# Optimization experiments

Hardware: AMD Instinct MI355X
Metric: run time of the kernel (lower is better)

## Reference

```python
import jax, jax.numpy as jnp
import numpy as np

N = 100000
E = 1600000
F_IN = 64
DIM = 64
OUT = 10
NUM_GRAPHS = 1000
BN_EPS = 1e-5


def gcn_conv(x, W, b, src, dst, n):
    # PyG GCNConv: add self-loops, symmetric normalization, scatter-add.
    h = x @ W                                   # [N, dim]
    ones = jnp.ones(src.shape[0], dtype=x.dtype)
    deg = jax.ops.segment_sum(ones, dst, num_segments=n) + 1.0  # +1 self-loop
    dinv = jax.lax.rsqrt(deg)                   # deg^{-1/2}
    msg = h[src] * (dinv[src] * dinv[dst])[:, None]  # [E, dim]
    out = jax.ops.segment_sum(msg, dst, num_segments=n)
    out = out + h * (dinv * dinv)[:, None]      # self-loop term
    return out + b


def batchnorm_eval(x, gamma, beta, mean, var):
    return (x - mean) * jax.lax.rsqrt(var + BN_EPS) * gamma + beta


def setup_inputs() -> dict:
    key = jax.random.key(0)
    ks = jax.random.split(key, 16)
    x = jax.random.normal(ks[0], (N, F_IN), dtype=jnp.float32)
    edge_index = jax.random.randint(ks[1], (2, E), 0, N)
    batch = jnp.sort(jax.random.randint(ks[2], (N,), 0, NUM_GRAPHS))

    def lin(k, fan_in, fan_out):
        s = 1.0 / np.sqrt(fan_in)
        kw, kb = jax.random.split(k)
        W = jax.random.uniform(kw, (fan_in, fan_out), minval=-s, maxval=s, dtype=jnp.float32)
        b = jax.random.uniform(kb, (fan_out,), minval=-s, maxval=s, dtype=jnp.float32)
        return W, b

    W1, b1 = lin(ks[3], F_IN, DIM)
    W2, b2 = lin(ks[4], DIM, DIM)
    W3, b3 = lin(ks[5], DIM, DIM)
    W4, b4 = lin(ks[6], DIM, DIM)
    lin1_W, lin1_b = lin(ks[7], 4 * DIM, DIM)
    lin2_W, lin2_b = lin(ks[8], DIM, OUT)

    bn_gamma = jnp.ones((4, DIM), dtype=jnp.float32)
    bn_beta = jnp.zeros((4, DIM), dtype=jnp.float32)
    bn_mean = jnp.zeros((4, DIM), dtype=jnp.float32)
    bn_var = jnp.ones((4, DIM), dtype=jnp.float32)

    return {
        'x': x, 'edge_index': edge_index, 'batch': batch, 'num_graphs': NUM_GRAPHS,
        'W1': W1, 'b1': b1, 'W2': W2, 'b2': b2, 'W3': W3, 'b3': b3, 'W4': W4, 'b4': b4,
        'bn_gamma': bn_gamma, 'bn_beta': bn_beta, 'bn_mean': bn_mean, 'bn_var': bn_var,
        'lin1_W': lin1_W, 'lin1_b': lin1_b, 'lin2_W': lin2_W, 'lin2_b': lin2_b,
    }


def reference(x, edge_index, batch, num_graphs, W1, b1, W2, b2, W3, b3, W4, b4,
              bn_gamma, bn_beta, bn_mean, bn_var, lin1_W, lin1_b, lin2_W, lin2_b):
    src, dst = edge_index[0], edge_index[1]
    n = x.shape[0]
    Ws = [(W1, b1), (W2, b2), (W3, b3), (W4, b4)]
    xs = []
    h = x
    for i, (W, b) in enumerate(Ws):
        h = gcn_conv(h, W, b, src, dst, n)
        h = batchnorm_eval(h, bn_gamma[i], bn_beta[i], bn_mean[i], bn_var[i])
        h = jax.nn.relu(h)
        xs.append(h)
    h = jnp.concatenate(xs, axis=-1)                         # JK 'cat' -> [N, 4*dim]
    pooled = jax.ops.segment_sum(h, batch, num_segments=num_graphs)  # [G, 4*dim]
    # dropout is identity in eval mode
    out = jax.nn.relu(pooled @ lin1_W + lin1_b)
    out = out @ lin2_W + lin2_b
    return out
```

## Files before the change

kernel.cpp:

```cpp
#include <hip/hip_runtime.h>
#include <hip/hip_bf16.h>

#define N_NODES   100000
#define N_EDGES   1600000
#define DIM       64
#define OUT_DIM   10
#define N_GRAPHS  1000
#define BN_EPS    1e-5f
#define NBUCKET   391
#define TILE_E    6400
#define NT        250

typedef __hip_bfloat16 bf16;
__device__ __forceinline__ float b2f(bf16 v) { return __bfloat162float(v); }

typedef __attribute__((ext_vector_type(8))) short short8;
typedef __attribute__((ext_vector_type(4))) float floatx4;

__device__ __forceinline__ short f2bs(float f) {
    union { bf16 h; short s; } u;
    u.h = __float2bfloat16(f);
    return u.s;
}


__global__ void __launch_bounds__(256) k_bucket_count(const int* __restrict__ dst,
                                                      int* __restrict__ tileCnt, int e) {
    __shared__ int hcnt[NBUCKET];
    int t = blockIdx.x, tid = threadIdx.x;
    for (int b = tid; b < NBUCKET; b += 256) hcnt[b] = 0;
    __syncthreads();
    int ibase = t * TILE_E;
    for (int j = 0; j < TILE_E; j += 256) {
        int i = ibase + j + tid;
        if (i < e) atomicAdd(&hcnt[dst[i] >> 8], 1);
    }
    __syncthreads();
    for (int b = tid; b < NBUCKET; b += 256) tileCnt[b * NT + t] = hcnt[b];
}


__global__ void __launch_bounds__(256) k_tile_scan(int* __restrict__ tileCnt,
                                                   int* __restrict__ bucketTot) {
    __shared__ int tmp[256];
    int b = blockIdx.x, tid = threadIdx.x;
    int v = (tid < NT) ? tileCnt[b * NT + tid] : 0;
    tmp[tid] = v;
    __syncthreads();
    for (int off = 1; off < 256; off <<= 1) {
        int t = (tid >= off) ? tmp[tid - off] : 0;
        __syncthreads();
        tmp[tid] += t;
        __syncthreads();
    }
    if (tid < NT) tileCnt[b * NT + tid] = tmp[tid] - v;
    if (tid == 255) bucketTot[b] = tmp[255];
}


__global__ void k_scan_sums(int* __restrict__ bsums, int nb) {
    __shared__ int tmp[512];
    int tid = threadIdx.x;
    int v = (tid < nb) ? bsums[tid] : 0;
    tmp[tid] = v;
    __syncthreads();
    for (int off = 1; off < 512; off <<= 1) {
        int t = (tid >= off) ? tmp[tid - off] : 0;
        __syncthreads();
        tmp[tid] += t;
        __syncthreads();
    }
    if (tid < nb) bsums[tid] = tmp[tid] - v;
}


__global__ void __launch_bounds__(256) k_bucket_write(
    const int* __restrict__ src, const int* __restrict__ dst,
    const int* __restrict__ bbase, const int* __restrict__ tilePrefix,
    unsigned int* __restrict__ packed, int e) {
    __shared__ int hbase[NBUCKET];
    __shared__ int hcur[NBUCKET];
    int t = blockIdx.x, tid = threadIdx.x;
    for (int b = tid; b < NBUCKET; b += 256) {
        hbase[b] = bbase[b] + tilePrefix[b * NT + t];
        hcur[b] = 0;
    }
    __syncthreads();
    int ibase = t * TILE_E;
    for (int j = 0; j < TILE_E; j += 256) {
        int i = ibase + j + tid;
        if (i < e) {
            int d  = dst[i];
            int bb = d >> 8;
            int pos = hbase[bb] + atomicAdd(&hcur[bb], 1);
            packed[pos] = ((unsigned int)src[i] << 8) | (unsigned int)(d & 255);
        }
    }
}


__global__ void __launch_bounds__(256) k_local_sort(
    const unsigned int* __restrict__ packed, const int* __restrict__ bbase,
    int* __restrict__ ssrc, int* __restrict__ offs, int* __restrict__ hist,
    float* __restrict__ dinv, int n, int e) {
    __shared__ int tmp[256];
    __shared__ int noffs[256];
    __shared__ int ncur[256];
    int b = blockIdx.x, tid = threadIdx.x;
    int base   = b << 8;
    int estart = bbase[b];
    int eend   = (b + 1 < NBUCKET) ? bbase[b + 1] : e;

    ncur[tid] = 0;
    __syncthreads();
    for (int i = estart + tid; i < eend; i += 256)
        atomicAdd(&ncur[packed[i] & 255u], 1);
    __syncthreads();
    int v = ncur[tid];
    tmp[tid] = v;
    __syncthreads();
    for (int off = 1; off < 256; off <<= 1) {
        int t = (tid >= off) ? tmp[tid - off] : 0;
        __syncthreads();
        tmp[tid] += t;
        __syncthreads();
    }
    int mystart = estart + tmp[tid] - v;
    noffs[tid] = mystart;
    ncur[tid]  = 0;
    int node = base + tid;
    if (node < n) {
        offs[node] = mystart;
        hist[node] = v;
        dinv[node] = rsqrtf((float)(v + 1));
    }
    __syncthreads();
    for (int i = estart + tid; i < eend; i += 256) {
        unsigned int p = packed[i];
        int d = p & 255u;
        int pos = noffs[d] + atomicAdd(&ncur[d], 1);
        ssrc[pos] = (int)(p >> 8);
    }
}


__global__ void __launch_bounds__(256) k_matmul_mfma(
    const float* __restrict__ hf, const float* __restrict__ W,
    const float* __restrict__ dinv, bf16* __restrict__ Hs, int ntiles, int nwaves)
{
    int wid  = (blockIdx.x * blockDim.x + threadIdx.x) >> 6;
    int lane = threadIdx.x & 63;
    if (wid >= ntiles) return;
    int quad = lane >> 4, m16 = lane & 15;

    short8 Bfrag[4][2];
#pragma unroll
    for (int t = 0; t < 4; t++)
#pragma unroll
        for (int h = 0; h < 2; h++) {
            short8 b;
#pragma unroll
            for (int j = 0; j < 8; j++)
                b[j] = f2bs(W[(h * 32 + quad * 8 + j) * 64 + t * 16 + m16]);
            Bfrag[t][h] = b;
        }

    for (int tile = wid; tile < ntiles; tile += nwaves) {
        int row0 = tile * 16;
        short8 A0, A1;
        const float* base = hf + (size_t)(row0 + m16) * 64 + quad * 8;
#pragma unroll
        for (int j = 0; j < 8; j++) {
            A0[j] = f2bs(base[j]);
            A1[j] = f2bs(base[32 + j]);
        }

        floatx4 acc[4];
#pragma unroll
        for (int t = 0; t < 4; t++) {
            floatx4 c = {0.f, 0.f, 0.f, 0.f};
            c = __builtin_amdgcn_mfma_f32_16x16x32_bf16(A0, Bfrag[t][0], c, 0, 0, 0);
            c = __builtin_amdgcn_mfma_f32_16x16x32_bf16(A1, Bfrag[t][1], c, 0, 0, 0);
            acc[t] = c;
        }

#pragma unroll
        for (int r = 0; r < 4; r++) {
            int row = row0 + quad * 4 + r;
            float dn = dinv[row];
#pragma unroll
            for (int t = 0; t < 4; t++)
                Hs[(size_t)row * 64 + t * 16 + m16] = __float2bfloat16(dn * acc[t][r]);
        }
    }
}


__global__ void __launch_bounds__(256) k_gather_mm(
    const bf16* __restrict__ HsIn, const int* __restrict__ ssrc,
    const int* __restrict__ offs, const int* __restrict__ hist,
    const float* __restrict__ dinv, const float* __restrict__ bias,
    const float* __restrict__ gamma, const float* __restrict__ beta,
    const float* __restrict__ mean, const float* __restrict__ var,
    const int* __restrict__ batch, const float* __restrict__ W,
    bf16* __restrict__ HsOut, float* __restrict__ pooled, int layer, int ntiles)
{
    __shared__ short tile[16][72];
    int wv   = threadIdx.x >> 6;
    int lane = threadIdx.x & 63;
    int quad = lane >> 4, m16 = lane & 15;

    float P = gamma[lane] * rsqrtf(var[lane] + BN_EPS);
    float Q = (bias[lane] - mean[lane]) * P + beta[lane];

    short8 B0, B1;
#pragma unroll
    for (int j = 0; j < 8; j++) {
        B0[j] = f2bs(W[(quad * 8 + j) * 64 + wv * 16 + m16]);
        B1[j] = f2bs(W[(32 + quad * 8 + j) * 64 + wv * 16 + m16]);
    }

    for (int t = blockIdx.x; t < ntiles; t += gridDim.x) {
        int row0 = t * 16;
#pragma unroll
        for (int j2 = 0; j2 < 4; j2++) {
            int node = row0 + wv * 4 + j2;
            int start = __builtin_amdgcn_readfirstlane(offs[node]);
            int cnt   = __builtin_amdgcn_readfirstlane(hist[node]);

            float acc = b2f(HsIn[node * 64 + lane]);
            int i = 0;
            for (; i + 15 < cnt; i += 16) {
                int s0  = ssrc[start + i];
                int s1  = ssrc[start + i + 1];
                int s2  = ssrc[start + i + 2];
                int s3  = ssrc[start + i + 3];
                int s4  = ssrc[start + i + 4];
                int s5  = ssrc[start + i + 5];
                int s6  = ssrc[start + i + 6];
                int s7  = ssrc[start + i + 7];
                int s8  = ssrc[start + i + 8];
                int s9  = ssrc[start + i + 9];
                int s10 = ssrc[start + i + 10];
                int s11 = ssrc[start + i + 11];
                int s12 = ssrc[start + i + 12];
                int s13 = ssrc[start + i + 13];
                int s14 = ssrc[start + i + 14];
                int s15 = ssrc[start + i + 15];
                float v0  = b2f(HsIn[s0  * 64 + lane]);
                float v1  = b2f(HsIn[s1  * 64 + lane]);
                float v2  = b2f(HsIn[s2  * 64 + lane]);
                float v3  = b2f(HsIn[s3  * 64 + lane]);
                float v4  = b2f(HsIn[s4  * 64 + lane]);
                float v5  = b2f(HsIn[s5  * 64 + lane]);
                float v6  = b2f(HsIn[s6  * 64 + lane]);
                float v7  = b2f(HsIn[s7  * 64 + lane]);
                float v8  = b2f(HsIn[s8  * 64 + lane]);
                float v9  = b2f(HsIn[s9  * 64 + lane]);
                float v10 = b2f(HsIn[s10 * 64 + lane]);
                float v11 = b2f(HsIn[s11 * 64 + lane]);
                float v12 = b2f(HsIn[s12 * 64 + lane]);
                float v13 = b2f(HsIn[s13 * 64 + lane]);
                float v14 = b2f(HsIn[s14 * 64 + lane]);
                float v15 = b2f(HsIn[s15 * 64 + lane]);
                acc += (((v0 + v1) + (v2 + v3)) + ((v4 + v5) + (v6 + v7))) +
                       (((v8 + v9) + (v10 + v11)) + ((v12 + v13) + (v14 + v15)));
            }
            for (; i + 3 < cnt; i += 4) {
                int s0 = ssrc[start + i];
                int s1 = ssrc[start + i + 1];
                int s2 = ssrc[start + i + 2];
                int s3 = ssrc[start + i + 3];
                float v0 = b2f(HsIn[s0 * 64 + lane]);
                float v1 = b2f(HsIn[s1 * 64 + lane]);
                float v2 = b2f(HsIn[s2 * 64 + lane]);
                float v3 = b2f(HsIn[s3 * 64 + lane]);
                acc += (v0 + v1) + (v2 + v3);
            }
            for (; i < cnt; i++)
                acc += b2f(HsIn[ssrc[start + i] * 64 + lane]);

            float val = fmaxf(dinv[node] * acc * P + Q, 0.f);
            atomicAdd(&pooled[batch[node] * 256 + layer * 64 + lane], val);
            tile[wv * 4 + j2][lane] = f2bs(val);
        }
        __syncthreads();

        short8 A0 = *(const short8*)&tile[m16][quad * 8];
        short8 A1 = *(const short8*)&tile[m16][32 + quad * 8];
        floatx4 c = {0.f, 0.f, 0.f, 0.f};
        c = __builtin_amdgcn_mfma_f32_16x16x32_bf16(A0, B0, c, 0, 0, 0);
        c = __builtin_amdgcn_mfma_f32_16x16x32_bf16(A1, B1, c, 0, 0, 0);
#pragma unroll
        for (int r = 0; r < 4; r++) {
            int row = row0 + quad * 4 + r;
            HsOut[(size_t)row * 64 + wv * 16 + m16] =
                __float2bfloat16(dinv[row] * c[r]);
        }
        __syncthreads();
    }
}


__global__ void __launch_bounds__(256) k_gather(
    const bf16* __restrict__ Hs, const int* __restrict__ ssrc,
    const int* __restrict__ offs, const int* __restrict__ hist,
    const float* __restrict__ dinv, const float* __restrict__ bias,
    const float* __restrict__ gamma, const float* __restrict__ beta,
    const float* __restrict__ mean, const float* __restrict__ var,
    const int* __restrict__ batch, float* __restrict__ pooled,
    int layer, int n, int nwaves)
{
    int wid  = (blockIdx.x * blockDim.x + threadIdx.x) >> 6;
    int lane = threadIdx.x & 63;

    float P = gamma[lane] * rsqrtf(var[lane] + BN_EPS);
    float Q = (bias[lane] - mean[lane]) * P + beta[lane];

    for (int node = wid; node < n; node += nwaves) {
        int start = __builtin_amdgcn_readfirstlane(offs[node]);
        int cnt   = __builtin_amdgcn_readfirstlane(hist[node]);

        float acc = b2f(Hs[node * 64 + lane]);
        int i = 0;
        for (; i + 15 < cnt; i += 16) {
            int s0  = ssrc[start + i];
            int s1  = ssrc[start + i + 1];
            int s2  = ssrc[start + i + 2];
            int s3  = ssrc[start + i + 3];
            int s4  = ssrc[start + i + 4];
            int s5  = ssrc[start + i + 5];
            int s6  = ssrc[start + i + 6];
            int s7  = ssrc[start + i + 7];
            int s8  = ssrc[start + i + 8];
            int s9  = ssrc[start + i + 9];
            int s10 = ssrc[start + i + 10];
            int s11 = ssrc[start + i + 11];
            int s12 = ssrc[start + i + 12];
            int s13 = ssrc[start + i + 13];
            int s14 = ssrc[start + i + 14];
            int s15 = ssrc[start + i + 15];
            float v0  = b2f(Hs[s0  * 64 + lane]);
            float v1  = b2f(Hs[s1  * 64 + lane]);
            float v2  = b2f(Hs[s2  * 64 + lane]);
            float v3  = b2f(Hs[s3  * 64 + lane]);
            float v4  = b2f(Hs[s4  * 64 + lane]);
            float v5  = b2f(Hs[s5  * 64 + lane]);
            float v6  = b2f(Hs[s6  * 64 + lane]);
            float v7  = b2f(Hs[s7  * 64 + lane]);
            float v8  = b2f(Hs[s8  * 64 + lane]);
            float v9  = b2f(Hs[s9  * 64 + lane]);
            float v10 = b2f(Hs[s10 * 64 + lane]);
            float v11 = b2f(Hs[s11 * 64 + lane]);
            float v12 = b2f(Hs[s12 * 64 + lane]);
            float v13 = b2f(Hs[s13 * 64 + lane]);
            float v14 = b2f(Hs[s14 * 64 + lane]);
            float v15 = b2f(Hs[s15 * 64 + lane]);
            acc += (((v0 + v1) + (v2 + v3)) + ((v4 + v5) + (v6 + v7))) +
                   (((v8 + v9) + (v10 + v11)) + ((v12 + v13) + (v14 + v15)));
        }
        for (; i + 7 < cnt; i += 8) {
            int s0 = ssrc[start + i];
            int s1 = ssrc[start + i + 1];
            int s2 = ssrc[start + i + 2];
            int s3 = ssrc[start + i + 3];
            int s4 = ssrc[start + i + 4];
            int s5 = ssrc[start + i + 5];
            int s6 = ssrc[start + i + 6];
            int s7 = ssrc[start + i + 7];
            float v0 = b2f(Hs[s0 * 64 + lane]);
            float v1 = b2f(Hs[s1 * 64 + lane]);
            float v2 = b2f(Hs[s2 * 64 + lane]);
            float v3 = b2f(Hs[s3 * 64 + lane]);
            float v4 = b2f(Hs[s4 * 64 + lane]);
            float v5 = b2f(Hs[s5 * 64 + lane]);
            float v6 = b2f(Hs[s6 * 64 + lane]);
            float v7 = b2f(Hs[s7 * 64 + lane]);
            acc += ((v0 + v1) + (v2 + v3)) + ((v4 + v5) + (v6 + v7));
        }
        for (; i + 3 < cnt; i += 4) {
            int s0 = ssrc[start + i];
            int s1 = ssrc[start + i + 1];
            int s2 = ssrc[start + i + 2];
            int s3 = ssrc[start + i + 3];
            float v0 = b2f(Hs[s0 * 64 + lane]);
            float v1 = b2f(Hs[s1 * 64 + lane]);
            float v2 = b2f(Hs[s2 * 64 + lane]);
            float v3 = b2f(Hs[s3 * 64 + lane]);
            acc += (v0 + v1) + (v2 + v3);
        }
        for (; i < cnt; i++)
            acc += b2f(Hs[ssrc[start + i] * 64 + lane]);

        float val = fmaxf(dinv[node] * acc * P + Q, 0.f);
        atomicAdd(&pooled[batch[node] * 256 + layer * 64 + lane], val);
    }
}


__global__ void k_mlp(const float* __restrict__ pooled, const float* __restrict__ W1,
                      const float* __restrict__ b1, const float* __restrict__ W2,
                      const float* __restrict__ b2, float* __restrict__ out) {
    __shared__ float p[256];
    __shared__ float t[64];
    int g = blockIdx.x;
    int tid = threadIdx.x;
    for (int i = tid; i < 256; i += 64) p[i] = pooled[g * 256 + i];
    __syncthreads();
    float acc = b1[tid];
    for (int k = 0; k < 256; k++)
        acc = fmaf(p[k], W1[k * 64 + tid], acc);
    t[tid] = fmaxf(acc, 0.f);
    __syncthreads();
    if (tid < OUT_DIM) {
        float o = b2[tid];
#pragma unroll
        for (int d = 0; d < 64; d++)
            o = fmaf(t[d], W2[d * OUT_DIM + tid], o);
        out[g * OUT_DIM + tid] = o;
    }
}


extern "C" void kernel_launch(void* const* d_in, const int* in_sizes, int n_in,
                              void* d_out, int out_size, void* d_ws, size_t ws_size,
                              hipStream_t stream) {
    const float* x          = (const float*)d_in[0];
    const int*   edge_index = (const int*)d_in[1];
    const int*   batch      = (const int*)d_in[2];
    const float* Wl[4] = { (const float*)d_in[4], (const float*)d_in[6],
                           (const float*)d_in[8], (const float*)d_in[10] };
    const float* bl[4] = { (const float*)d_in[5], (const float*)d_in[7],
                           (const float*)d_in[9], (const float*)d_in[11] };
    const float* bn_gamma = (const float*)d_in[12];
    const float* bn_beta  = (const float*)d_in[13];
    const float* bn_mean  = (const float*)d_in[14];
    const float* bn_var   = (const float*)d_in[15];
    const float* lin1_W = (const float*)d_in[16];
    const float* lin1_b = (const float*)d_in[17];
    const float* lin2_W = (const float*)d_in[18];
    const float* lin2_b = (const float*)d_in[19];

    const int* src = edge_index;
    const int* dst = edge_index + N_EDGES;

    char* p = (char*)d_ws;
    auto alloc = [&](size_t bytes) {
        char* r = p;
        p += (bytes + 255) & ~(size_t)255;
        return (void*)r;
    };
    bf16*  HsA    = (bf16*) alloc((size_t)N_NODES * 64 * 2);
    bf16*  HsB    = (bf16*) alloc((size_t)N_NODES * 64 * 2);
    int*   hist   = (int*)  alloc((size_t)N_NODES * 4);
    int*   offs   = (int*)  alloc((size_t)N_NODES * 4);
    float* dinv   = (float*)alloc((size_t)N_NODES * 4);
    int*   ssrc   = (int*)  alloc((size_t)N_EDGES * 4);
    unsigned int* packed = (unsigned int*)alloc((size_t)N_EDGES * 4);
    int*   tileCnt   = (int*)alloc((size_t)NBUCKET * NT * 4);
    int*   bucketTot = (int*)alloc((size_t)NBUCKET * 4);
    float* pooled = (float*)alloc((size_t)N_GRAPHS * 256 * 4);

    hipMemsetAsync(pooled, 0, (size_t)N_GRAPHS * 256 * 4, stream);

    k_bucket_count<<<NT, 256, 0, stream>>>(dst, tileCnt, N_EDGES);
    k_tile_scan<<<NBUCKET, 256, 0, stream>>>(tileCnt, bucketTot);
    k_scan_sums<<<1, 512, 0, stream>>>(bucketTot, NBUCKET);
    k_bucket_write<<<NT, 256, 0, stream>>>(src, dst, bucketTot, tileCnt, packed, N_EDGES);
    k_local_sort<<<NBUCKET, 256, 0, stream>>>(packed, bucketTot, ssrc, offs, hist,
                                              dinv, N_NODES, N_EDGES);

    const int mmTiles  = N_NODES / 16;
    const int mmBlocks = 512;
    const int mmWaves  = mmBlocks * 4;

    k_matmul_mfma<<<mmBlocks, 256, 0, stream>>>(x, Wl[0], dinv, HsA, mmTiles, mmWaves);

    bf16* hsIn[3]  = { HsA, HsB, HsA };
    bf16* hsOut[3] = { HsB, HsA, HsB };
    for (int layer = 0; layer < 3; layer++) {
        k_gather_mm<<<2048, 256, 0, stream>>>(
            hsIn[layer], ssrc, offs, hist, dinv, bl[layer],
            bn_gamma + layer * 64, bn_beta + layer * 64,
            bn_mean + layer * 64, bn_var + layer * 64,
            batch, Wl[layer + 1], hsOut[layer], pooled, layer, mmTiles);
    }
    k_gather<<<4096, 256, 0, stream>>>(
        HsB, ssrc, offs, hist, dinv, bl[3],
        bn_gamma + 3 * 64, bn_beta + 3 * 64,
        bn_mean + 3 * 64, bn_var + 3 * 64,
        batch, pooled, 3, N_NODES, 4096 * 4);

    k_mlp<<<N_GRAPHS, 64, 0, stream>>>(pooled, lin1_W, lin1_b, lin2_W, lin2_b,
                                       (float*)d_out);
}
```

Before: 441.0 us.

## Give each wave a full tile in gather_mm, stage W in LDS, pre-reduce pooling

The fused gather+matmul kernel now assigns a whole 16-node tile to each wave, which drops the block-wide __syncthreads. The layer weight is staged once per block in LDS in MFMA fragment order, and each wave computes all four output column tiles. Pooling atomics in both gather kernels are pre-reduced per wave across consecutive nodes of the same graph, using contiguous node chunks in the last gather. The pooled memset is folded into the bucket-count kernel. The risks are less parallelism per tile, longer serial per-wave work and more LDS use per block.

Result: no change. 448.9 us (+1.8%).

```diff
diff --git a/kernel.cpp b/kernel.cpp
--- a/kernel.cpp
+++ b/kernel.cpp
@@ -25,10 +25,12 @@
 
 
 __global__ void __launch_bounds__(256) k_bucket_count(const int* __restrict__ dst,
-                                                      int* __restrict__ tileCnt, int e) {
+                                                      int* __restrict__ tileCnt,
+                                                      float* __restrict__ pooled, int e) {
     __shared__ int hcnt[NBUCKET];
     int t = blockIdx.x, tid = threadIdx.x;
     for (int b = tid; b < NBUCKET; b += 256) hcnt[b] = 0;
+    for (int i = t * 256 + tid; i < N_GRAPHS * 256; i += NT * 256) pooled[i] = 0.f;
     __syncthreads();
     int ibase = t * TILE_E;
     for (int j = 0; j < TILE_E; j += 256) {
@@ -150,7 +152,6 @@
 {
     int wid  = (blockIdx.x * blockDim.x + threadIdx.x) >> 6;
     int lane = threadIdx.x & 63;
-    if (wid >= ntiles) return;
     int quad = lane >> 4, m16 = lane & 15;
 
     short8 Bfrag[4][2];
@@ -203,28 +204,35 @@
     const float* __restrict__ gamma, const float* __restrict__ beta,
     const float* __restrict__ mean, const float* __restrict__ var,
     const int* __restrict__ batch, const float* __restrict__ W,
-    bf16* __restrict__ HsOut, float* __restrict__ pooled, int layer, int ntiles)
+    bf16* __restrict__ HsOut, float* __restrict__ pooled, int layer,
+    int ntiles, int nwaves)
 {
-    __shared__ short tile[16][72];
-    int wv   = threadIdx.x >> 6;
-    int lane = threadIdx.x & 63;
+    __shared__ short Wlds[4096];
+    __shared__ short tile[4][16][72];
+    int tid  = threadIdx.x;
+    int wv   = tid >> 6;
+    int lane = tid & 63;
     int quad = lane >> 4, m16 = lane & 15;
+
+    for (int e = tid; e < 4096; e += 256) {
+        int j = e & 7, idx = e >> 3;
+        int em16 = idx & 15, equad = (idx >> 4) & 3, eh = (idx >> 6) & 1, et = idx >> 7;
+        Wlds[e] = f2bs(W[(eh * 32 + equad * 8 + j) * 64 + et * 16 + em16]);
+    }
+    __syncthreads();
 
     float P = gamma[lane] * rsqrtf(var[lane] + BN_EPS);
     float Q = (bias[lane] - mean[lane]) * P + beta[lane];
 
-    short8 B0, B1;
-#pragma unroll
-    for (int j = 0; j < 8; j++) {
-        B0[j] = f2bs(W[(quad * 8 + j) * 64 + wv * 16 + m16]);
-        B1[j] = f2bs(W[(32 + quad * 8 + j) * 64 + wv * 16 + m16]);
-    }
-
-    for (int t = blockIdx.x; t < ntiles; t += gridDim.x) {
-        int row0 = t * 16;
-#pragma unroll
-        for (int j2 = 0; j2 < 4; j2++) {
-            int node = row0 + wv * 4 + j2;
+    int wid = (blockIdx.x * blockDim.x + tid) >> 6;
+
+    for (int t0 = wid; t0 < ntiles; t0 += nwaves) {
+        int row0 = t0 * 16;
+        float pacc = 0.f;
+        int   curg = -1;
+
+        for (int j2 = 0; j2 < 16; j2++) {
+            int node  = row0 + j2;
             int start = __builtin_amdgcn_readfirstlane(offs[node]);
             int cnt   = __builtin_amdgcn_readfirstlane(hist[node]);
 
@@ -266,6 +274,25 @@
                 acc += (((v0 + v1) + (v2 + v3)) + ((v4 + v5) + (v6 + v7))) +
                        (((v8 + v9) + (v10 + v11)) + ((v12 + v13) + (v14 + v15)));
             }
+            for (; i + 7 < cnt; i += 8) {
+                int s0 = ssrc[start + i];
+                int s1 = ssrc[start + i + 1];
+                int s2 = ssrc[start + i + 2];
+                int s3 = ssrc[start + i + 3];
+                int s4 = ssrc[start + i + 4];
+                int s5 = ssrc[start + i + 5];
+                int s6 = ssrc[start + i + 6];
+                int s7 = ssrc[start + i + 7];
+                float v0 = b2f(HsIn[s0 * 64 + lane]);
+                float v1 = b2f(HsIn[s1 * 64 + lane]);
+                float v2 = b2f(HsIn[s2 * 64 + lane]);
+                float v3 = b2f(HsIn[s3 * 64 + lane]);
+                float v4 = b2f(HsIn[s4 * 64 + lane]);
+                float v5 = b2f(HsIn[s5 * 64 + lane]);
+                float v6 = b2f(HsIn[s6 * 64 + lane]);
+                float v7 = b2f(HsIn[s7 * 64 + lane]);
+                acc += ((v0 + v1) + (v2 + v3)) + ((v4 + v5) + (v6 + v7));
+            }
             for (; i + 3 < cnt; i += 4) {
                 int s0 = ssrc[start + i];
                 int s1 = ssrc[start + i + 1];
@@ -281,23 +308,37 @@
                 acc += b2f(HsIn[ssrc[start + i] * 64 + lane]);
 
             float val = fmaxf(dinv[node] * acc * P + Q, 0.f);
-            atomicAdd(&pooled[batch[node] * 256 + layer * 64 + lane], val);
-            tile[wv * 4 + j2][lane] = f2bs(val);
-        }
-        __syncthreads();
-
-        short8 A0 = *(const short8*)&tile[m16][quad * 8];
-        short8 A1 = *(const short8*)&tile[m16][32 + quad * 8];
-        floatx4 c = {0.f, 0.f, 0.f, 0.f};
-        c = __builtin_amdgcn_mfma_f32_16x16x32_bf16(A0, B0, c, 0, 0, 0);
-        c = __builtin_amdgcn_mfma_f32_16x16x32_bf16(A1, B1, c, 0, 0, 0);
-#pragma unroll
-        for (int r = 0; r < 4; r++) {
-            int row = row0 + quad * 4 + r;
-            HsOut[(size_t)row * 64 + wv * 16 + m16] =
-                __float2bfloat16(dinv[row] * c[r]);
-        }
-        __syncthreads();
+
+            int g = __builtin_amdgcn_readfirstlane(batch[node]);
+            if (g != curg) {
+                if (curg >= 0)
+                    atomicAdd(&pooled[curg * 256 + layer * 64 + lane], pacc);
+                pacc = 0.f;
+                curg = g;
+            }
+            pacc += val;
+
+            tile[wv][j2][lane] = f2bs(val);
+        }
+        if (curg >= 0)
+            atomicAdd(&pooled[curg * 256 + layer * 64 + lane], pacc);
+
+        short8 A0 = *(const short8*)&tile[wv][m16][quad * 8];
+        short8 A1 = *(const short8*)&tile[wv][m16][32 + quad * 8];
+#pragma unroll
+        for (int t = 0; t < 4; t++) {
+            short8 B0 = *(const short8*)&Wlds[(((t * 2 + 0) * 4 + quad) * 16 + m16) * 8];
+            short8 B1 = *(const short8*)&Wlds[(((t * 2 + 1) * 4 + quad) * 16 + m16) * 8];
+            floatx4 c = {0.f, 0.f, 0.f, 0.f};
+            c = __builtin_amdgcn_mfma_f32_16x16x32_bf16(A0, B0, c, 0, 0, 0);
+            c = __builtin_amdgcn_mfma_f32_16x16x32_bf16(A1, B1, c, 0, 0, 0);
+#pragma unroll
+            for (int r = 0; r < 4; r++) {
+                int row = row0 + quad * 4 + r;
+                HsOut[(size_t)row * 64 + t * 16 + m16] =
+                    __float2bfloat16(dinv[row] * c[r]);
+            }
+        }
     }
 }
 
@@ -317,7 +358,14 @@
     float P = gamma[lane] * rsqrtf(var[lane] + BN_EPS);
     float Q = (bias[lane] - mean[lane]) * P + beta[lane];
 
-    for (int node = wid; node < n; node += nwaves) {
+    int chunk = (n + nwaves - 1) / nwaves;
+    int node0 = wid * chunk;
+    int node1 = min(node0 + chunk, n);
+
+    float pacc = 0.f;
+    int   curg = -1;
+
+    for (int node = node0; node < node1; node++) {
         int start = __builtin_amdgcn_readfirstlane(offs[node]);
         int cnt   = __builtin_amdgcn_readfirstlane(hist[node]);
 
@@ -393,8 +441,18 @@
             acc += b2f(Hs[ssrc[start + i] * 64 + lane]);
 
         float val = fmaxf(dinv[node] * acc * P + Q, 0.f);
-        atomicAdd(&pooled[batch[node] * 256 + layer * 64 + lane], val);
-    }
+
+        int g = __builtin_amdgcn_readfirstlane(batch[node]);
+        if (g != curg) {
+            if (curg >= 0)
+                atomicAdd(&pooled[curg * 256 + layer * 64 + lane], pacc);
+            pacc = 0.f;
+            curg = g;
+        }
+        pacc += val;
+    }
+    if (curg >= 0)
+        atomicAdd(&pooled[curg * 256 + layer * 64 + lane], pacc);
 }
 
 
@@ -461,9 +519,7 @@
     int*   bucketTot = (int*)alloc((size_t)NBUCKET * 4);
     float* pooled = (float*)alloc((size_t)N_GRAPHS * 256 * 4);
 
-    hipMemsetAsync(pooled, 0, (size_t)N_GRAPHS * 256 * 4, stream);
-
-    k_bucket_count<<<NT, 256, 0, stream>>>(dst, tileCnt, N_EDGES);
+    k_bucket_count<<<NT, 256, 0, stream>>>(dst, tileCnt, pooled, N_EDGES);
     k_tile_scan<<<NBUCKET, 256, 0, stream>>>(tileCnt, bucketTot);
     k_scan_sums<<<1, 512, 0, stream>>>(bucketTot, NBUCKET);
     k_bucket_write<<<NT, 256, 0, stream>>>(src, dst, bucketTot, tileCnt, packed, N_EDGES);
@@ -476,14 +532,16 @@
 
     k_matmul_mfma<<<mmBlocks, 256, 0, stream>>>(x, Wl[0], dinv, HsA, mmTiles, mmWaves);
 
+    const int fBlocks = (mmTiles + 3) / 4;
+    const int fWaves  = fBlocks * 4;
     bf16* hsIn[3]  = { HsA, HsB, HsA };
     bf16* hsOut[3] = { HsB, HsA, HsB };
     for (int layer = 0; layer < 3; layer++) {
-        k_gather_mm<<<2048, 256, 0, stream>>>(
+        k_gather_mm<<<fBlocks, 256, 0, stream>>>(
             hsIn[layer], ssrc, offs, hist, dinv, bl[layer],
             bn_gamma + layer * 64, bn_beta + layer * 64,
             bn_mean + layer * 64, bn_var + layer * 64,
-            batch, Wl[layer + 1], hsOut[layer], pooled, layer, mmTiles);
+            batch, Wl[layer + 1], hsOut[layer], pooled, layer, mmTiles, fWaves);
     }
     k_gather<<<4096, 256, 0, stream>>>(
         HsB, ssrc, offs, hist, dinv, bl[3],
```
